# Optimization experiments

Measured on AMD Instinct MI355X. Metric: run time of the kernel, lower is better.

Reference implementation:

```python
import jax, jax.numpy as jnp
import numpy as np
import math

N = 30000
E = 600000
IN_DIM = 256
HID = 64
EMB = 64
HEADS = 4
EPS = 1e-5


def _glorot(key, shape):
    fan_in, fan_out = shape[0], shape[1]
    lim = math.sqrt(6.0 / (fan_in + fan_out))
    return jax.random.uniform(key, shape, jnp.float32, -lim, lim)


def setup_inputs() -> dict:
    key = jax.random.key(0)
    ks = jax.random.split(key, 24)
    inp = {
        "x": jax.random.normal(ks[0], (N, IN_DIM), jnp.float32),
        "edge_index": jax.random.randint(ks[1], (2, E), 0, N, jnp.int64),
    }
    # layer 1: in=IN_DIM, out per head=HID, heads=HEADS -> width HID*HEADS
    w1 = HID * HEADS
    inp.update({
        "w1q": _glorot(ks[2], (IN_DIM, w1)), "b1q": jnp.zeros((w1,), jnp.float32),
        "w1k": _glorot(ks[3], (IN_DIM, w1)), "b1k": jnp.zeros((w1,), jnp.float32),
        "w1v": _glorot(ks[4], (IN_DIM, w1)), "b1v": jnp.zeros((w1,), jnp.float32),
        "w1s": _glorot(ks[5], (IN_DIM, w1)), "b1s": jnp.zeros((w1,), jnp.float32),
        "g1": jnp.ones((w1,), jnp.float32), "be1": jnp.zeros((w1,), jnp.float32),
    })
    # layer 2: in=HID*HEADS, out per head=EMB -> width EMB*HEADS
    w2 = EMB * HEADS
    inp.update({
        "w2q": _glorot(ks[6], (w1, w2)), "b2q": jnp.zeros((w2,), jnp.float32),
        "w2k": _glorot(ks[7], (w1, w2)), "b2k": jnp.zeros((w2,), jnp.float32),
        "w2v": _glorot(ks[8], (w1, w2)), "b2v": jnp.zeros((w2,), jnp.float32),
        "w2s": _glorot(ks[9], (w1, w2)), "b2s": jnp.zeros((w2,), jnp.float32),
        "g2": jnp.ones((w2,), jnp.float32), "be2": jnp.zeros((w2,), jnp.float32),
    })
    return inp


def transformer_conv(x, edge_index, wq, bq, wk, bk, wv, bv, ws, bs, heads, out_ch):
    n = x.shape[0]
    q = (x @ wq + bq).reshape(n, heads, out_ch)
    k = (x @ wk + bk).reshape(n, heads, out_ch)
    v = (x @ wv + bv).reshape(n, heads, out_ch)
    src, dst = edge_index[0], edge_index[1]
    # per-edge gather: [E, H, C]
    qi, kj, vj = q[dst], k[src], v[src]
    alpha = jnp.sum(qi * kj, axis=-1) / math.sqrt(out_ch)  # [E, H]
    # segment softmax over incoming edges of each target node
    amax = jax.lax.stop_gradient(jax.ops.segment_max(alpha, dst, num_segments=n))
    ex = jnp.exp(alpha - amax[dst])
    denom = jax.ops.segment_sum(ex, dst, num_segments=n)
    alpha = ex / denom[dst]
    # scatter-add weighted values back to targets
    out = jax.ops.segment_sum(vj * alpha[..., None], dst, num_segments=n)
    out = out.reshape(n, heads * out_ch)
    return out + x @ ws + bs  # root/skip connection


def batch_norm(x, gamma, beta):
    mean = jnp.mean(x, axis=0)
    var = jnp.mean(jnp.square(x - mean), axis=0)  # biased, training-mode BN
    return (x - mean) * jax.lax.rsqrt(var + EPS) * gamma + beta


def leaky_relu(x):
    return jnp.where(x >= 0, x, 0.1 * x)


def reference(x, edge_index, w1q, b1q, w1k, b1k, w1v, b1v, w1s, b1s, g1, be1,
              w2q, b2q, w2k, b2k, w2v, b2v, w2s, b2s, g2, be2):
    h = transformer_conv(x, edge_index, w1q, b1q, w1k, b1k, w1v, b1v, w1s, b1s, HEADS, HID)
    h = leaky_relu(batch_norm(h, g1, be1))
    h = transformer_conv(h, edge_index, w2q, b2q, w2k, b2k, w2v, b2v, w2s, b2s, HEADS, EMB)
    h = leaky_relu(batch_norm(h, g2, be2))
    return h
```

## Files before the change

### kernel.cpp

```cpp
#include <hip/hip_runtime.h>
#include <math.h>

#define NODES 30000
#define EDGES 600000
#define QKVS_W 1024
#define OUT_W 256
#define BN_EPS 1e-5f

typedef __attribute__((ext_vector_type(8))) __bf16 bf16x8;
typedef __attribute__((ext_vector_type(4))) float f32x4;

__device__ __forceinline__ unsigned short f2bf(float f) {
    union { float f; unsigned int u; } v; v.f = f;
    unsigned int r = v.u + 0x7FFFu + ((v.u >> 16) & 1u);
    return (unsigned short)(r >> 16);
}
__device__ __forceinline__ float bf2f(unsigned short u) {
    union { unsigned int u; float f; } v; v.u = ((unsigned int)u) << 16;
    return v.f;
}

typedef const __attribute__((address_space(1))) void* gas_p;
typedef __attribute__((address_space(3))) void* las_p;
__device__ __forceinline__ void gload_lds16(const void* g, void* l) {
    __builtin_amdgcn_global_load_lds((gas_p)g, (las_p)l, 16, 0, 0);
}


__global__ __launch_bounds__(256) void k_count(const int* __restrict__ ei, int* __restrict__ deg) {
    int e = blockIdx.x * 256 + threadIdx.x;
    if (e < EDGES) atomicAdd(&deg[ei[EDGES + e]], 1);
}

__global__ __launch_bounds__(256) void k_blocksum(const int* __restrict__ deg, int* __restrict__ bsum) {
    __shared__ int sh[256];
    int i = blockIdx.x * 256 + threadIdx.x;
    sh[threadIdx.x] = (i < NODES) ? deg[i] : 0;
    __syncthreads();
    for (int off = 128; off > 0; off >>= 1) {
        if (threadIdx.x < off) sh[threadIdx.x] += sh[threadIdx.x + off];
        __syncthreads();
    }
    if (threadIdx.x == 0) bsum[blockIdx.x] = sh[0];
}

__global__ __launch_bounds__(128) void k_scanb(const int* __restrict__ bsum, int* __restrict__ bbase, int nb) {
    __shared__ int sh[128];
    int t = threadIdx.x;
    int v = (t < nb) ? bsum[t] : 0;
    sh[t] = v;
    __syncthreads();
    for (int off = 1; off < 128; off <<= 1) {
        int add = (t >= off) ? sh[t - off] : 0;
        __syncthreads();
        sh[t] += add;
        __syncthreads();
    }
    if (t < nb) bbase[t] = sh[t] - v;
}

__global__ __launch_bounds__(256) void k_localscan(const int* __restrict__ deg, const int* __restrict__ bbase,
                                                   int* __restrict__ rowptr, int* __restrict__ cursor) {
    __shared__ int sh[256];
    int i = blockIdx.x * 256 + threadIdx.x;
    int v = (i < NODES) ? deg[i] : 0;
    sh[threadIdx.x] = v;
    __syncthreads();
    for (int off = 1; off < 256; off <<= 1) {
        int add = (threadIdx.x >= off) ? sh[threadIdx.x - off] : 0;
        __syncthreads();
        sh[threadIdx.x] += add;
        __syncthreads();
    }
    if (i < NODES) {
        int p = bbase[blockIdx.x] + sh[threadIdx.x] - v;
        rowptr[i] = p;
        cursor[i] = p;
    }
}

__global__ __launch_bounds__(256) void k_fill(const int* __restrict__ ei, int* __restrict__ cursor,
                                              int* __restrict__ csr_src) {
    int e = blockIdx.x * 256 + threadIdx.x;
    if (e < EDGES) {
        int s = ei[e];
        int d = ei[EDGES + e];
        int slot = atomicAdd(&cursor[d], 1);
        csr_src[slot] = s;
    }
}


__global__ __launch_bounds__(256) void k_castA(const float* __restrict__ in, unsigned short* __restrict__ out, int n8) {
    int i = blockIdx.x * 256 + threadIdx.x;
    if (i >= n8) return;
    const float4* p = (const float4*)(in + (size_t)i * 8);
    float4 v0 = p[0], v1 = p[1];
    ushort4 o0, o1;
    o0.x = f2bf(v0.x); o0.y = f2bf(v0.y); o0.z = f2bf(v0.z); o0.w = f2bf(v0.w);
    o1.x = f2bf(v1.x); o1.y = f2bf(v1.y); o1.z = f2bf(v1.z); o1.w = f2bf(v1.w);
    ushort4* q = (ushort4*)(out + (size_t)i * 8);
    q[0] = o0; q[1] = o1;
}

__global__ __launch_bounds__(256) void k_castW2(
    const float* __restrict__ Wa0, const float* __restrict__ Wa1,
    const float* __restrict__ Wa2, const float* __restrict__ Wa3,
    const float* __restrict__ Ba0, const float* __restrict__ Ba1,
    const float* __restrict__ Ba2, const float* __restrict__ Ba3,
    const float* __restrict__ Wb0, const float* __restrict__ Wb1,
    const float* __restrict__ Wb2, const float* __restrict__ Wb3,
    const float* __restrict__ Bb0, const float* __restrict__ Bb1,
    const float* __restrict__ Bb2, const float* __restrict__ Bb3,
    unsigned short* __restrict__ Wt1, float* __restrict__ bf1,
    unsigned short* __restrict__ Wt2, float* __restrict__ bf2)
{
    int nn0 = blockIdx.x;
    int layer = nn0 >> 10;
    int n = nn0 & 1023;
    int k = threadIdx.x;
    int wsel = n >> 8, nc = n & 255;
    const float* W; const float* Bv;
    if (layer == 0) {
        W  = (wsel == 0) ? Wa0 : (wsel == 1) ? Wa1 : (wsel == 2) ? Wa2 : Wa3;
        Bv = (wsel == 0) ? Ba0 : (wsel == 1) ? Ba1 : (wsel == 2) ? Ba2 : Ba3;
    } else {
        W  = (wsel == 0) ? Wb0 : (wsel == 1) ? Wb1 : (wsel == 2) ? Wb2 : Wb3;
        Bv = (wsel == 0) ? Bb0 : (wsel == 1) ? Bb1 : (wsel == 2) ? Bb2 : Bb3;
    }
    unsigned short* Wt = (layer == 0) ? Wt1 : Wt2;
    float* bfused = (layer == 0) ? bf1 : bf2;
    Wt[(size_t)n * 256 + k] = f2bf(W[(size_t)k * 256 + nc]);
    if (k == 0) bfused[n] = Bv[nc];
}


#define CS 136

__global__ __launch_bounds__(256) void k_gemm_bf16(
    const unsigned short* __restrict__ A,
    const unsigned short* __restrict__ Wt,
    const float* __restrict__ bias,
    unsigned short* __restrict__ C, int M)
{
    __shared__ unsigned short sbuf[128 * CS];
    unsigned short* As = sbuf;
    unsigned short* Bs = sbuf + 8192;
    int tid = threadIdx.x;
    int lane = tid & 63;
    int wave = tid >> 6;
    int wm = wave & 1, wn = wave >> 1;
    int row0 = blockIdx.x * 128;
    int n0 = blockIdx.y * 128;

    f32x4 acc[4][4] = {};

    for (int k0 = 0; k0 < 256; k0 += 64) {
        #pragma unroll
        for (int w = 0; w < 4; w++) {
            int c = w * 256 + tid;
            int row = c >> 3;
            int cole = (c & 7) * 8;
            int ar = row0 + row; if (ar >= M) ar = M - 1;
            gload_lds16(&A[(size_t)ar * 256 + k0 + cole], &As[w * 2048 + tid * 8]);
            gload_lds16(&Wt[(size_t)(n0 + row) * 256 + k0 + cole], &Bs[w * 2048 + tid * 8]);
        }
        __syncthreads();
        int rsel = lane & 15;
        int kq = (lane >> 4) * 8;
        #pragma unroll
        for (int kh = 0; kh < 2; kh++) {
            bf16x8 af[4], bf[4];
            #pragma unroll
            for (int t = 0; t < 4; t++) {
                af[t] = *reinterpret_cast<const bf16x8*>(&As[(wm * 64 + t * 16 + rsel) * 64 + kh * 32 + kq]);
                bf[t] = *reinterpret_cast<const bf16x8*>(&Bs[(wn * 64 + t * 16 + rsel) * 64 + kh * 32 + kq]);
            }
            #pragma unroll
            for (int mt = 0; mt < 4; mt++)
                #pragma unroll
                for (int nt = 0; nt < 4; nt++)
                    acc[mt][nt] = __builtin_amdgcn_mfma_f32_16x16x32_bf16(af[mt], bf[nt], acc[mt][nt], 0, 0, 0);
        }
        __syncthreads();
    }

    int crow = (lane >> 4) * 4;
    int ccol = lane & 15;
    #pragma unroll
    for (int mt = 0; mt < 4; mt++) {
        int lrow = wm * 64 + mt * 16 + crow;
        #pragma unroll
        for (int nt = 0; nt < 4; nt++) {
            int lcol = wn * 64 + nt * 16 + ccol;
            float bv = bias[n0 + lcol];
            #pragma unroll
            for (int r = 0; r < 4; r++)
                sbuf[(lrow + r) * CS + lcol] = f2bf(acc[mt][nt][r] + bv);
        }
    }
    __syncthreads();
    int chunk = tid & 15;
    int rbase = tid >> 4;
    #pragma unroll
    for (int g = 0; g < 8; g++) {
        int row_l = g * 16 + rbase;
        int gr = row0 + row_l;
        if (gr < M) {
            uint4 val = *(const uint4*)&sbuf[row_l * CS + chunk * 8];
            *(uint4*)&C[(size_t)gr * QKVS_W + n0 + chunk * 8] = val;
        }
    }
}


__global__ __launch_bounds__(256) void k_attn_bf16(const unsigned short* __restrict__ qkvs,
                                                   const int* __restrict__ rowptr,
                                                   const int* __restrict__ deg,
                                                   const int* __restrict__ csr_src,
                                                   float* __restrict__ out)
{
    int wave = threadIdx.x >> 6;
    int lane = threadIdx.x & 63;
    int node = blockIdx.x * 4 + wave;
    if (node >= NODES) return;

    const unsigned short* qrow = qkvs + (size_t)node * QKVS_W;
    float q0, q1, q2, q3;
    {
        ushort4 qv = *(const ushort4*)&qrow[lane * 4];
        q0 = bf2f(qv.x); q1 = bf2f(qv.y); q2 = bf2f(qv.z); q3 = bf2f(qv.w);
    }

    float m = -INFINITY, L = 0.f;
    float a0 = 0.f, a1 = 0.f, a2 = 0.f, a3 = 0.f;

    int start = rowptr[node];
    int cnt = deg[node];

    ushort4 kA, vA, kB, vB;
    if (cnt > 0) {
        const unsigned short* p = qkvs + (size_t)csr_src[start] * QKVS_W;
        kA = *(const ushort4*)&p[256 + lane * 4];
        vA = *(const ushort4*)&p[512 + lane * 4];
    }
    if (cnt > 1) {
        const unsigned short* p = qkvs + (size_t)csr_src[start + 1] * QKVS_W;
        kB = *(const ushort4*)&p[256 + lane * 4];
        vB = *(const ushort4*)&p[512 + lane * 4];
    }
    int e = 0;
    for (; e + 1 < cnt; e += 2) {
        ushort4 nkA, nvA, nkB, nvB;
        if (e + 2 < cnt) {
            const unsigned short* p = qkvs + (size_t)csr_src[start + e + 2] * QKVS_W;
            nkA = *(const ushort4*)&p[256 + lane * 4];
            nvA = *(const ushort4*)&p[512 + lane * 4];
        }
        if (e + 3 < cnt) {
            const unsigned short* p = qkvs + (size_t)csr_src[start + e + 3] * QKVS_W;
            nkB = *(const ushort4*)&p[256 + lane * 4];
            nvB = *(const ushort4*)&p[512 + lane * 4];
        }
        float d1 = q0 * bf2f(kA.x) + q1 * bf2f(kA.y) + q2 * bf2f(kA.z) + q3 * bf2f(kA.w);
        float d2 = q0 * bf2f(kB.x) + q1 * bf2f(kB.y) + q2 * bf2f(kB.z) + q3 * bf2f(kB.w);
        d1 += __shfl_xor(d1, 1, 64);  d2 += __shfl_xor(d2, 1, 64);
        d1 += __shfl_xor(d1, 2, 64);  d2 += __shfl_xor(d2, 2, 64);
        d1 += __shfl_xor(d1, 4, 64);  d2 += __shfl_xor(d2, 4, 64);
        d1 += __shfl_xor(d1, 8, 64);  d2 += __shfl_xor(d2, 8, 64);
        float al1 = d1 * 0.125f;
        float al2 = d2 * 0.125f;
        float nm = fmaxf(m, fmaxf(al1, al2));
        float sc = __expf(m - nm);
        float p1 = __expf(al1 - nm);
        float p2 = __expf(al2 - nm);
        L  = L * sc + p1 + p2;
        a0 = a0 * sc + p1 * bf2f(vA.x) + p2 * bf2f(vB.x);
        a1 = a1 * sc + p1 * bf2f(vA.y) + p2 * bf2f(vB.y);
        a2 = a2 * sc + p1 * bf2f(vA.z) + p2 * bf2f(vB.z);
        a3 = a3 * sc + p1 * bf2f(vA.w) + p2 * bf2f(vB.w);
        m = nm;
        kA = nkA; vA = nvA; kB = nkB; vB = nvB;
    }
    if (e < cnt) {
        float d1 = q0 * bf2f(kA.x) + q1 * bf2f(kA.y) + q2 * bf2f(kA.z) + q3 * bf2f(kA.w);
        d1 += __shfl_xor(d1, 1, 64);
        d1 += __shfl_xor(d1, 2, 64);
        d1 += __shfl_xor(d1, 4, 64);
        d1 += __shfl_xor(d1, 8, 64);
        float al1 = d1 * 0.125f;
        float nm = fmaxf(m, al1);
        float sc = __expf(m - nm);
        float p1 = __expf(al1 - nm);
        L  = L * sc + p1;
        a0 = a0 * sc + p1 * bf2f(vA.x);
        a1 = a1 * sc + p1 * bf2f(vA.y);
        a2 = a2 * sc + p1 * bf2f(vA.z);
        a3 = a3 * sc + p1 * bf2f(vA.w);
    }

    float inv = (L > 0.f) ? 1.f / L : 0.f;
    ushort4 sv = *(const ushort4*)&qrow[768 + lane * 4];
    float4 o;
    o.x = a0 * inv + bf2f(sv.x);
    o.y = a1 * inv + bf2f(sv.y);
    o.z = a2 * inv + bf2f(sv.z);
    o.w = a3 * inv + bf2f(sv.w);
    *(float4*)&out[(size_t)node * OUT_W + lane * 4] = o;
}


__global__ __launch_bounds__(256) void k_bnstats(const float* __restrict__ h,
                                                 float* __restrict__ sum, float* __restrict__ sumsq) {
    int col = threadIdx.x;
    int r0 = blockIdx.x * 64;
    int r1 = min(r0 + 64, NODES);
    float s = 0.f, s2 = 0.f;
    for (int r = r0; r < r1; r++) {
        float v = h[(size_t)r * OUT_W + col];
        s += v; s2 += v * v;
    }
    atomicAdd(&sum[col], s);
    atomicAdd(&sumsq[col], s2);
}

__device__ __forceinline__ float4 bn_scale4(const float* sum, const float* sumsq,
                                            const float* g, const float* be,
                                            int col, float4* shift) {
    float4 s  = *(const float4*)&sum[col];
    float4 s2 = *(const float4*)&sumsq[col];
    float4 gv = *(const float4*)&g[col];
    float4 bv = *(const float4*)&be[col];
    const float invN = 1.0f / NODES;
    float4 sc, sh;
    float mean, var;
    mean = s.x * invN; var = fmaxf(s2.x * invN - mean * mean, 0.f);
    sc.x = gv.x * rsqrtf(var + BN_EPS); sh.x = bv.x - mean * sc.x;
    mean = s.y * invN; var = fmaxf(s2.y * invN - mean * mean, 0.f);
    sc.y = gv.y * rsqrtf(var + BN_EPS); sh.y = bv.y - mean * sc.y;
    mean = s.z * invN; var = fmaxf(s2.z * invN - mean * mean, 0.f);
    sc.z = gv.z * rsqrtf(var + BN_EPS); sh.z = bv.z - mean * sc.z;
    mean = s.w * invN; var = fmaxf(s2.w * invN - mean * mean, 0.f);
    sc.w = gv.w * rsqrtf(var + BN_EPS); sh.w = bv.w - mean * sc.w;
    *shift = sh;
    return sc;
}

__global__ __launch_bounds__(256) void k_bnapply_bf16(const float* __restrict__ h,
                                                      const float* __restrict__ sum,
                                                      const float* __restrict__ sumsq,
                                                      const float* __restrict__ g,
                                                      const float* __restrict__ be,
                                                      unsigned short* __restrict__ out) {
    int idx = blockIdx.x * 256 + threadIdx.x;
    int base = idx * 4;
    int col = base & (OUT_W - 1);
    float4 sh;
    float4 sc = bn_scale4(sum, sumsq, g, be, col, &sh);
    float4 v = *(const float4*)&h[base];
    float4 o;
    o.x = v.x * sc.x + sh.x; o.x = (o.x >= 0.f) ? o.x : 0.1f * o.x;
    o.y = v.y * sc.y + sh.y; o.y = (o.y >= 0.f) ? o.y : 0.1f * o.y;
    o.z = v.z * sc.z + sh.z; o.z = (o.z >= 0.f) ? o.z : 0.1f * o.z;
    o.w = v.w * sc.w + sh.w; o.w = (o.w >= 0.f) ? o.w : 0.1f * o.w;
    ushort4 u; u.x = f2bf(o.x); u.y = f2bf(o.y); u.z = f2bf(o.z); u.w = f2bf(o.w);
    *(ushort4*)&out[base] = u;
}

__global__ __launch_bounds__(256) void k_bnapply(const float* __restrict__ h,
                                                 const float* __restrict__ sum,
                                                 const float* __restrict__ sumsq,
                                                 const float* __restrict__ g,
                                                 const float* __restrict__ be,
                                                 float* __restrict__ out) {
    int idx = blockIdx.x * 256 + threadIdx.x;
    int base = idx * 4;
    int col = base & (OUT_W - 1);
    float4 sh;
    float4 sc = bn_scale4(sum, sumsq, g, be, col, &sh);
    float4 v = *(const float4*)&h[base];
    float4 o;
    o.x = v.x * sc.x + sh.x; o.x = (o.x >= 0.f) ? o.x : 0.1f * o.x;
    o.y = v.y * sc.y + sh.y; o.y = (o.y >= 0.f) ? o.y : 0.1f * o.y;
    o.z = v.z * sc.z + sh.z; o.z = (o.z >= 0.f) ? o.z : 0.1f * o.z;
    o.w = v.w * sc.w + sh.w; o.w = (o.w >= 0.f) ? o.w : 0.1f * o.w;
    *(float4*)&out[base] = o;
}


extern "C" void kernel_launch(void* const* d_in, const int* in_sizes, int n_in,
                              void* d_out, int out_size, void* d_ws, size_t ws_size,
                              hipStream_t stream) {
    const float* x  = (const float*)d_in[0];
    const int*   ei = (const int*)d_in[1];
    const float* w1[4] = {(const float*)d_in[2], (const float*)d_in[4], (const float*)d_in[6], (const float*)d_in[8]};
    const float* b1[4] = {(const float*)d_in[3], (const float*)d_in[5], (const float*)d_in[7], (const float*)d_in[9]};
    const float* g1  = (const float*)d_in[10];
    const float* be1 = (const float*)d_in[11];
    const float* w2[4] = {(const float*)d_in[12], (const float*)d_in[14], (const float*)d_in[16], (const float*)d_in[18]};
    const float* b2[4] = {(const float*)d_in[13], (const float*)d_in[15], (const float*)d_in[17], (const float*)d_in[19]};
    const float* g2  = (const float*)d_in[20];
    const float* be2 = (const float*)d_in[21];

    char* ws = (char*)d_ws;
    unsigned short* qkvsb  = (unsigned short*)(ws);
    float*          h1     = (float*)(ws + 61440000);
    unsigned short* abuf   = (unsigned short*)(ws + 92160000);
    unsigned short* wt1    = (unsigned short*)(ws + 107520000);
    unsigned short* wt2    = (unsigned short*)(ws + 108044288);
    float*          b1f    = (float*)(ws + 108568576);
    float*          b2f    = (float*)(ws + 108572672);
    int*            deg    = (int*)  (ws + 108576768);
    int*            rowptr = (int*)  (ws + 108696768);
    int*            cursor = (int*)  (ws + 108816768);
    int*            csr    = (int*)  (ws + 108936768);
    int*            bsum   = (int*)  (ws + 111336768);
    int*            bbase  = (int*)  (ws + 111337280);
    float*          sum1   = (float*)(ws + 111337792);
    float*          sq1    = (float*)(ws + 111338816);
    float*          sum2   = (float*)(ws + 111339840);
    float*          sq2    = (float*)(ws + 111340864);

    hipMemsetAsync(deg, 0, NODES * sizeof(int), stream);
    hipMemsetAsync(sum1, 0, 4096, stream);

    const int EB = (EDGES + 255) / 256;
    const int NB = (NODES + 255) / 256;

    k_castA<<<(NODES * 256 / 8 + 255) / 256, 256, 0, stream>>>(x, abuf, NODES * 256 / 8);
    k_castW2<<<2048, 256, 0, stream>>>(w1[0], w1[1], w1[2], w1[3], b1[0], b1[1], b1[2], b1[3],
                                       w2[0], w2[1], w2[2], w2[3], b2[0], b2[1], b2[2], b2[3],
                                       wt1, b1f, wt2, b2f);

    k_count    <<<EB, 256, 0, stream>>>(ei, deg);
    k_blocksum <<<NB, 256, 0, stream>>>(deg, bsum);
    k_scanb    <<<1, 128, 0, stream>>>(bsum, bbase, NB);
    k_localscan<<<NB, 256, 0, stream>>>(deg, bbase, rowptr, cursor);
    k_fill     <<<EB, 256, 0, stream>>>(ei, cursor, csr);

    dim3 ggrid((NODES + 127) / 128, 8);
    const int ANB = NODES / 4;
    const int APB = (NODES * OUT_W / 4) / 256;
    const int SNB = (NODES + 63) / 64;

    k_gemm_bf16  <<<ggrid, 256, 0, stream>>>(abuf, wt1, b1f, qkvsb, NODES);
    k_attn_bf16  <<<ANB, 256, 0, stream>>>(qkvsb, rowptr, deg, csr, h1);
    k_bnstats    <<<SNB, 256, 0, stream>>>(h1, sum1, sq1);
    k_bnapply_bf16<<<APB, 256, 0, stream>>>(h1, sum1, sq1, g1, be1, abuf);

    k_gemm_bf16  <<<ggrid, 256, 0, stream>>>(abuf, wt2, b2f, qkvsb, NODES);
    k_attn_bf16  <<<ANB, 256, 0, stream>>>(qkvsb, rowptr, deg, csr, h1);
    k_bnstats    <<<SNB, 256, 0, stream>>>(h1, sum2, sq2);
    k_bnapply    <<<APB, 256, 0, stream>>>(h1, sum2, sq2, g2, be2, (float*)d_out);
}
```

Before: 517.7 us.

## Store attention output in bf16 and fold memsets and block-sum into existing kernels

```diff
diff --git a/kernel.cpp b/kernel.cpp
--- a/kernel.cpp
+++ b/kernel.cpp
@@ -32,23 +32,16 @@
     if (e < EDGES) atomicAdd(&deg[ei[EDGES + e]], 1);
 }
 
-__global__ __launch_bounds__(256) void k_blocksum(const int* __restrict__ deg, int* __restrict__ bsum) {
-    __shared__ int sh[256];
-    int i = blockIdx.x * 256 + threadIdx.x;
-    sh[threadIdx.x] = (i < NODES) ? deg[i] : 0;
-    __syncthreads();
-    for (int off = 128; off > 0; off >>= 1) {
-        if (threadIdx.x < off) sh[threadIdx.x] += sh[threadIdx.x + off];
-        __syncthreads();
-    }
-    if (threadIdx.x == 0) bsum[blockIdx.x] = sh[0];
-}
-
-__global__ __launch_bounds__(128) void k_scanb(const int* __restrict__ bsum, int* __restrict__ bbase, int nb) {
+__global__ __launch_bounds__(128) void k_degscan(const int* __restrict__ deg, int* __restrict__ bbase, int nb) {
     __shared__ int sh[128];
     int t = threadIdx.x;
-    int v = (t < nb) ? bsum[t] : 0;
-    sh[t] = v;
+    int s = 0;
+    if (t < nb) {
+        int base = t * 256;
+        int end = min(base + 256, NODES);
+        for (int i = base; i < end; i++) s += deg[i];
+    }
+    sh[t] = s;
     __syncthreads();
     for (int off = 1; off < 128; off <<= 1) {
         int add = (t >= off) ? sh[t - off] : 0;
@@ -56,7 +49,7 @@
         sh[t] += add;
         __syncthreads();
     }
-    if (t < nb) bbase[t] = sh[t] - v;
+    if (t < nb) bbase[t] = sh[t] - s;
 }
 
 __global__ __launch_bounds__(256) void k_localscan(const int* __restrict__ deg, const int* __restrict__ bbase,
@@ -91,8 +84,11 @@
 }
 
 
-__global__ __launch_bounds__(256) void k_castA(const float* __restrict__ in, unsigned short* __restrict__ out, int n8) {
+__global__ __launch_bounds__(256) void k_castA(const float* __restrict__ in, unsigned short* __restrict__ out,
+                                               int n8, int* __restrict__ deg, float* __restrict__ sums) {
     int i = blockIdx.x * 256 + threadIdx.x;
+    if (i < NODES) deg[i] = 0;
+    if (i < 1024) sums[i] = 0.f;
     if (i >= n8) return;
     const float4* p = (const float4*)(in + (size_t)i * 8);
     float4 v0 = p[0], v1 = p[1];
@@ -218,7 +214,7 @@
                                                    const int* __restrict__ rowptr,
                                                    const int* __restrict__ deg,
                                                    const int* __restrict__ csr_src,
-                                                   float* __restrict__ out)
+                                                   unsigned short* __restrict__ out)
 {
     int wave = threadIdx.x >> 6;
     int lane = threadIdx.x & 63;
@@ -301,23 +297,23 @@
 
     float inv = (L > 0.f) ? 1.f / L : 0.f;
     ushort4 sv = *(const ushort4*)&qrow[768 + lane * 4];
-    float4 o;
-    o.x = a0 * inv + bf2f(sv.x);
-    o.y = a1 * inv + bf2f(sv.y);
-    o.z = a2 * inv + bf2f(sv.z);
-    o.w = a3 * inv + bf2f(sv.w);
-    *(float4*)&out[(size_t)node * OUT_W + lane * 4] = o;
-}
-
-
-__global__ __launch_bounds__(256) void k_bnstats(const float* __restrict__ h,
+    ushort4 u;
+    u.x = f2bf(a0 * inv + bf2f(sv.x));
+    u.y = f2bf(a1 * inv + bf2f(sv.y));
+    u.z = f2bf(a2 * inv + bf2f(sv.z));
+    u.w = f2bf(a3 * inv + bf2f(sv.w));
+    *(ushort4*)&out[(size_t)node * OUT_W + lane * 4] = u;
+}
+
+
+__global__ __launch_bounds__(256) void k_bnstats(const unsigned short* __restrict__ h,
                                                  float* __restrict__ sum, float* __restrict__ sumsq) {
     int col = threadIdx.x;
     int r0 = blockIdx.x * 64;
     int r1 = min(r0 + 64, NODES);
     float s = 0.f, s2 = 0.f;
     for (int r = r0; r < r1; r++) {
-        float v = h[(size_t)r * OUT_W + col];
+        float v = bf2f(h[(size_t)r * OUT_W + col]);
         s += v; s2 += v * v;
     }
     atomicAdd(&sum[col], s);
@@ -346,7 +342,7 @@
     return sc;
 }
 
-__global__ __launch_bounds__(256) void k_bnapply_bf16(const float* __restrict__ h,
+__global__ __launch_bounds__(256) void k_bnapply_bf16(const unsigned short* __restrict__ h,
                                                       const float* __restrict__ sum,
                                                       const float* __restrict__ sumsq,
                                                       const float* __restrict__ g,
@@ -357,17 +353,17 @@
     int col = base & (OUT_W - 1);
     float4 sh;
     float4 sc = bn_scale4(sum, sumsq, g, be, col, &sh);
-    float4 v = *(const float4*)&h[base];
+    ushort4 hv = *(const ushort4*)&h[base];
     float4 o;
-    o.x = v.x * sc.x + sh.x; o.x = (o.x >= 0.f) ? o.x : 0.1f * o.x;
-    o.y = v.y * sc.y + sh.y; o.y = (o.y >= 0.f) ? o.y : 0.1f * o.y;
-    o.z = v.z * sc.z + sh.z; o.z = (o.z >= 0.f) ? o.z : 0.1f * o.z;
-    o.w = v.w * sc.w + sh.w; o.w = (o.w >= 0.f) ? o.w : 0.1f * o.w;
+    o.x = bf2f(hv.x) * sc.x + sh.x; o.x = (o.x >= 0.f) ? o.x : 0.1f * o.x;
+    o.y = bf2f(hv.y) * sc.y + sh.y; o.y = (o.y >= 0.f) ? o.y : 0.1f * o.y;
+    o.z = bf2f(hv.z) * sc.z + sh.z; o.z = (o.z >= 0.f) ? o.z : 0.1f * o.z;
+    o.w = bf2f(hv.w) * sc.w + sh.w; o.w = (o.w >= 0.f) ? o.w : 0.1f * o.w;
     ushort4 u; u.x = f2bf(o.x); u.y = f2bf(o.y); u.z = f2bf(o.z); u.w = f2bf(o.w);
     *(ushort4*)&out[base] = u;
 }
 
-__global__ __launch_bounds__(256) void k_bnapply(const float* __restrict__ h,
+__global__ __launch_bounds__(256) void k_bnapply(const unsigned short* __restrict__ h,
                                                  const float* __restrict__ sum,
                                                  const float* __restrict__ sumsq,
                                                  const float* __restrict__ g,
@@ -378,12 +374,12 @@
     int col = base & (OUT_W - 1);
     float4 sh;
     float4 sc = bn_scale4(sum, sumsq, g, be, col, &sh);
-    float4 v = *(const float4*)&h[base];
+    ushort4 hv = *(const ushort4*)&h[base];
     float4 o;
-    o.x = v.x * sc.x + sh.x; o.x = (o.x >= 0.f) ? o.x : 0.1f * o.x;
-    o.y = v.y * sc.y + sh.y; o.y = (o.y >= 0.f) ? o.y : 0.1f * o.y;
-    o.z = v.z * sc.z + sh.z; o.z = (o.z >= 0.f) ? o.z : 0.1f * o.z;
-    o.w = v.w * sc.w + sh.w; o.w = (o.w >= 0.f) ? o.w : 0.1f * o.w;
+    o.x = bf2f(hv.x) * sc.x + sh.x; o.x = (o.x >= 0.f) ? o.x : 0.1f * o.x;
+    o.y = bf2f(hv.y) * sc.y + sh.y; o.y = (o.y >= 0.f) ? o.y : 0.1f * o.y;
+    o.z = bf2f(hv.z) * sc.z + sh.z; o.z = (o.z >= 0.f) ? o.z : 0.1f * o.z;
+    o.w = bf2f(hv.w) * sc.w + sh.w; o.w = (o.w >= 0.f) ? o.w : 0.1f * o.w;
     *(float4*)&out[base] = o;
 }
 
@@ -404,37 +400,32 @@
 
     char* ws = (char*)d_ws;
     unsigned short* qkvsb  = (unsigned short*)(ws);
-    float*          h1     = (float*)(ws + 61440000);
-    unsigned short* abuf   = (unsigned short*)(ws + 92160000);
-    unsigned short* wt1    = (unsigned short*)(ws + 107520000);
-    unsigned short* wt2    = (unsigned short*)(ws + 108044288);
-    float*          b1f    = (float*)(ws + 108568576);
-    float*          b2f    = (float*)(ws + 108572672);
-    int*            deg    = (int*)  (ws + 108576768);
-    int*            rowptr = (int*)  (ws + 108696768);
-    int*            cursor = (int*)  (ws + 108816768);
-    int*            csr    = (int*)  (ws + 108936768);
-    int*            bsum   = (int*)  (ws + 111336768);
-    int*            bbase  = (int*)  (ws + 111337280);
-    float*          sum1   = (float*)(ws + 111337792);
-    float*          sq1    = (float*)(ws + 111338816);
-    float*          sum2   = (float*)(ws + 111339840);
-    float*          sq2    = (float*)(ws + 111340864);
-
-    hipMemsetAsync(deg, 0, NODES * sizeof(int), stream);
-    hipMemsetAsync(sum1, 0, 4096, stream);
+    unsigned short* h1     = (unsigned short*)(ws + 61440000);
+    unsigned short* abuf   = (unsigned short*)(ws + 76800000);
+    unsigned short* wt1    = (unsigned short*)(ws + 92160000);
+    unsigned short* wt2    = (unsigned short*)(ws + 92684288);
+    float*          b1f    = (float*)(ws + 93208576);
+    float*          b2f    = (float*)(ws + 93212672);
+    int*            deg    = (int*)  (ws + 93216768);
+    int*            rowptr = (int*)  (ws + 93336768);
+    int*            cursor = (int*)  (ws + 93456768);
+    int*            csr    = (int*)  (ws + 93576768);
+    int*            bbase  = (int*)  (ws + 95976768);
+    float*          sum1   = (float*)(ws + 95977280);
+    float*          sq1    = (float*)(ws + 95978304);
+    float*          sum2   = (float*)(ws + 95979328);
+    float*          sq2    = (float*)(ws + 95980352);
 
     const int EB = (EDGES + 255) / 256;
     const int NB = (NODES + 255) / 256;
 
-    k_castA<<<(NODES * 256 / 8 + 255) / 256, 256, 0, stream>>>(x, abuf, NODES * 256 / 8);
+    k_castA<<<(NODES * 256 / 8 + 255) / 256, 256, 0, stream>>>(x, abuf, NODES * 256 / 8, deg, sum1);
     k_castW2<<<2048, 256, 0, stream>>>(w1[0], w1[1], w1[2], w1[3], b1[0], b1[1], b1[2], b1[3],
                                        w2[0], w2[1], w2[2], w2[3], b2[0], b2[1], b2[2], b2[3],
                                        wt1, b1f, wt2, b2f);
 
     k_count    <<<EB, 256, 0, stream>>>(ei, deg);
-    k_blocksum <<<NB, 256, 0, stream>>>(deg, bsum);
-    k_scanb    <<<1, 128, 0, stream>>>(bsum, bbase, NB);
+    k_degscan  <<<1, 128, 0, stream>>>(deg, bbase, NB);
     k_localscan<<<NB, 256, 0, stream>>>(deg, bbase, rowptr, cursor);
     k_fill     <<<EB, 256, 0, stream>>>(ei, cursor, csr);
 
```

New measurement: 524.1 us. No clear change (+1.2%).
